# Performance work log

Hardware: AMD Instinct MI355X
Metric: run time of the kernel (lower is better)

The kernel has to match this reference:

```python
import jax, jax.numpy as jnp
import numpy as np
from jax import lax

B, H, W = 8, 2048, 2048

def _conv3x3(x, w):
    # x: [B,H,W,1], w: [3,3,1,1] (HWIO), SAME padding, stride 1
    return lax.conv_general_dilated(
        x, w, window_strides=(1, 1), padding='SAME',
        dimension_numbers=('NHWC', 'HWIO', 'NHWC'))

def setup_inputs() -> dict:
    key = jax.random.key(0)
    k1, k2, k3, k4, k5, k6 = jax.random.split(key, 6)
    x = jax.random.normal(k1, (B, H, W, 1), dtype=jnp.float32)
    mask = jax.random.randint(k2, (B, H, W, 1), 0, 2, dtype=jnp.int32)
    w1 = jax.random.normal(k3, (3, 3, 1, 1), dtype=jnp.float32)
    b1 = jax.random.normal(k4, (1,), dtype=jnp.float32)
    w2 = jax.random.normal(k5, (3, 3, 1, 1), dtype=jnp.float32)
    b2 = jax.random.normal(k6, (1,), dtype=jnp.float32)
    return {"x": x, "mask": mask, "w1": w1, "b1": b1, "w2": w2, "b2": b2}

def reference(x, mask, w1, b1, w2, b2):
    # Stride-1 MinkowskiConvolution on a sparse 2D tensor == dense 3x3 conv over
    # features zeroed at unoccupied coords, with bias + output restricted to the
    # occupied coordinate set (out_coords == in_coords for stride 1).
    m = mask.astype(x.dtype)                       # occupancy [B,H,W,1]
    h = (_conv3x3(x * m, w1) + b1) * m             # conv1 + bias on active coords
    h = jax.nn.relu(h)                             # MinkowskiReLU (per active coord)
    out = (_conv3x3(h, w2) + b2) * m               # conv2 + bias on active coords
    return out
```

## Files before the change

### kernel.cpp

```cpp
#include <hip/hip_runtime.h>


#define TB_W 128
#define TB_H 16
#define SX   136
#define SY   20
#define NV4  (SX / 4)
#define NSTG (SY * NV4)
#define HR   18
#define NQR  33
#define NQ   (HR * NQR)
#define IMG_W 2048
#define IMG_H 2048

__global__ __launch_bounds__(256) void fused_mconv2(
    const float* __restrict__ x, const int* __restrict__ mask,
    const float* __restrict__ w1p, const float* __restrict__ b1p,
    const float* __restrict__ w2p, const float* __restrict__ b2p,
    float* __restrict__ out)
{
    __shared__ __align__(16) float s_xm[SY][SX];
    __shared__ __align__(16) float s_hm[HR][SX];
    __shared__ __align__(4)  unsigned char s_mb[HR][SX];

    const int hw   = (blockIdx.z * gridDim.y + blockIdx.y) * gridDim.x + blockIdx.x;
    const int xcd  = hw & 7;
    const int slot = hw >> 3;
    const int orig = (xcd << 11) + slot;
    const int ty   = orig & 127;
    const int cl   = orig >> 7;
    const int tx   = cl & 15;
    const int tz   = cl >> 4;

    const int tid  = threadIdx.y * 64 + threadIdx.x;
    const int c0   = tx * TB_W;
    const int row0 = ty * TB_H;
    const size_t plane = (size_t)IMG_W * IMG_H;
    const float* xb = x    + (size_t)tz * plane;
    const int*   mb = mask + (size_t)tz * plane;
    float*       ob = out  + (size_t)tz * plane;

    float W1[9], W2[9];
    #pragma unroll
    for (int i = 0; i < 9; ++i) { W1[i] = w1p[i]; W2[i] = w2p[i]; }
    const float B1 = b1p[0], B2 = b2p[0];

    for (int idx = tid; idx < NSTG; idx += 256) {
        const int row  = idx / NV4;
        const int col4 = idx - row * NV4;
        const int r = row0 - 2 + row;
        const int c = c0 - 4 + (col4 << 2);
        float4 xm = make_float4(0.f, 0.f, 0.f, 0.f);
        unsigned mpack = 0u;
        if (r >= 0 && r < IMG_H && c >= 0 && c < IMG_W) {
            const size_t g = (size_t)r * IMG_W + c;
            const float4 xv = *reinterpret_cast<const float4*>(xb + g);
            const int4   mi = *reinterpret_cast<const int4*>(mb + g);
            xm.x = mi.x ? xv.x : 0.f;
            xm.y = mi.y ? xv.y : 0.f;
            xm.z = mi.z ? xv.z : 0.f;
            xm.w = mi.w ? xv.w : 0.f;
            mpack = (mi.x ? 1u : 0u) | (mi.y ? 256u : 0u) |
                    (mi.z ? 65536u : 0u) | (mi.w ? 16777216u : 0u);
        }
        *reinterpret_cast<float4*>(&s_xm[row][col4 << 2]) = xm;
        if (row >= 1 && row <= HR)
            *reinterpret_cast<unsigned*>(&s_mb[row - 1][col4 << 2]) = mpack;
    }
    __syncthreads();

    for (int idx = tid; idx < NQ; idx += 256) {
        const int hr = idx / NQR;
        const int q  = idx - hr * NQR;
        const int hc = q << 2;
        float a0 = B1, a1 = B1, a2 = B1, a3 = B1;
        #pragma unroll
        for (int di = 0; di < 3; ++di) {
            const float4 A  = *reinterpret_cast<const float4*>(&s_xm[hr + di][hc]);
            const float4 Bv = *reinterpret_cast<const float4*>(&s_xm[hr + di][hc + 4]);
            const float w0 = W1[di * 3], w1 = W1[di * 3 + 1], w2 = W1[di * 3 + 2];
            a0 += w0 * A.z  + w1 * A.w  + w2 * Bv.x;
            a1 += w0 * A.w  + w1 * Bv.x + w2 * Bv.y;
            a2 += w0 * Bv.x + w1 * Bv.y + w2 * Bv.z;
            a3 += w0 * Bv.y + w1 * Bv.z + w2 * Bv.w;
        }
        const unsigned mA = *reinterpret_cast<const unsigned*>(&s_mb[hr][hc]);
        const unsigned mB = *reinterpret_cast<const unsigned*>(&s_mb[hr][hc + 4]);
        float4 e;
        e.x = ((mA >> 24) & 255u) ? fmaxf(a0, 0.f) : -1.0f;
        e.y = ( mB        & 255u) ? fmaxf(a1, 0.f) : -1.0f;
        e.z = ((mB >>  8) & 255u) ? fmaxf(a2, 0.f) : -1.0f;
        e.w = ((mB >> 16) & 255u) ? fmaxf(a3, 0.f) : -1.0f;
        *reinterpret_cast<float4*>(&s_hm[hr][hc]) = e;
    }
    __syncthreads();

    {
        const int j     = tid & 127;
        const int strip = tid >> 7;
        const int i0    = strip * (TB_H / 2);
        float P = 0.f, Q = 0.f, cm = 0.f;
        #pragma unroll
        for (int t = 0; t < TB_H / 2 + 2; ++t) {
            const int hr = i0 + t;
            const float* rowp = &s_hm[hr][0];
            const float t0 = rowp[j];
            const float t1 = rowp[j + 1];
            const float t2 = rowp[j + 2];
            const float r0 = t0 > 0.f ? t0 : 0.f;
            const float r1 = t1 > 0.f ? t1 : 0.f;
            const float r2 = t2 > 0.f ? t2 : 0.f;
            const float d0 = W2[0] * r0 + W2[1] * r1 + W2[2] * r2;
            const float d1 = W2[3] * r0 + W2[4] * r1 + W2[5] * r2;
            const float d2 = W2[6] * r0 + W2[7] * r1 + W2[8] * r2;
            if (t >= 2) {
                const int i = i0 + t - 2;
                const float v = (cm >= 0.f) ? (Q + d2 + B2) : 0.f;
                __builtin_nontemporal_store(
                    v, ob + (size_t)(row0 + i) * IMG_W + (c0 + j));
            }
            Q  = P + d1;
            P  = d0;
            cm = t1;
        }
    }
}

extern "C" void kernel_launch(void* const* d_in, const int* in_sizes, int n_in,
                              void* d_out, int out_size, void* d_ws, size_t ws_size,
                              hipStream_t stream) {
    const float* x    = (const float*)d_in[0];
    const int*   mask = (const int*)  d_in[1];
    const float* w1   = (const float*)d_in[2];
    const float* b1   = (const float*)d_in[3];
    const float* w2   = (const float*)d_in[4];
    const float* b2   = (const float*)d_in[5];
    float*       out  = (float*)d_out;

    dim3 block(64, 4, 1);
    dim3 grid(IMG_W / TB_W, IMG_H / TB_H, 8);
    hipLaunchKernelGGL(fused_mconv2, grid, block, 0, stream,
                       x, mask, w1, b1, w2, b2, out);
}
```

Before: 72.81 us.

## Process two row bands per block with register-prefetched loads overlapping compute

Each block now handles two vertically adjacent 16-row tiles. The global loads for the second tile are issued into registers before the first tile's conv1 runs, so memory latency overlaps with compute. Shared buffers are doubled, the grid is halved to a 1D launch with XCD-aware remapping, and loads use clamped addresses so they can be issued without branching. This costs more LDS and registers per block, which may reduce occupancy, and it still reloads the halo rows shared by the two tiles.

```diff
diff --git a/kernel.cpp b/kernel.cpp
--- a/kernel.cpp
+++ b/kernel.cpp
@@ -19,22 +19,23 @@
     const float* __restrict__ w2p, const float* __restrict__ b2p,
     float* __restrict__ out)
 {
-    __shared__ __align__(16) float s_xm[SY][SX];
-    __shared__ __align__(16) float s_hm[HR][SX];
-    __shared__ __align__(4)  unsigned char s_mb[HR][SX];
+    __shared__ __align__(16) float s_xm0[SY][SX], s_xm1[SY][SX];
+    __shared__ __align__(16) float s_hm0[HR][SX], s_hm1[HR][SX];
+    __shared__ __align__(4)  unsigned char s_mb0[HR][SX], s_mb1[HR][SX];
 
-    const int hw   = (blockIdx.z * gridDim.y + blockIdx.y) * gridDim.x + blockIdx.x;
+    const int hw   = blockIdx.x;
     const int xcd  = hw & 7;
     const int slot = hw >> 3;
-    const int orig = (xcd << 11) + slot;
-    const int ty   = orig & 127;
-    const int cl   = orig >> 7;
+    const int orig = (xcd << 10) + slot;
+    const int band = orig & 63;
+    const int cl   = orig >> 6;
     const int tx   = cl & 15;
     const int tz   = cl >> 4;
 
     const int tid  = threadIdx.y * 64 + threadIdx.x;
     const int c0   = tx * TB_W;
-    const int row0 = ty * TB_H;
+    const int r0A  = band * (2 * TB_H);
+    const int r0B  = r0A + TB_H;
     const size_t plane = (size_t)IMG_W * IMG_H;
     const float* xb = x    + (size_t)tz * plane;
     const int*   mb = mask + (size_t)tz * plane;
@@ -45,57 +46,83 @@
     for (int i = 0; i < 9; ++i) { W1[i] = w1p[i]; W2[i] = w2p[i]; }
     const float B1 = b1p[0], B2 = b2p[0];
 
-    for (int idx = tid; idx < NSTG; idx += 256) {
-        const int row  = idx / NV4;
-        const int col4 = idx - row * NV4;
-        const int r = row0 - 2 + row;
-        const int c = c0 - 4 + (col4 << 2);
-        float4 xm = make_float4(0.f, 0.f, 0.f, 0.f);
-        unsigned mpack = 0u;
-        if (r >= 0 && r < IMG_H && c >= 0 && c < IMG_W) {
+    float4 xrA[3]; int4 mrA[3];
+    float4 xrB[3]; int4 mrB[3];
+    auto issue_loads = [&](int r0t, float4* xr, int4* mr) {
+        #pragma unroll
+        for (int u = 0; u < 3; ++u) {
+            const int idx  = tid + (u << 8);
+            const int cidx = idx < NSTG ? idx : NSTG - 1;
+            const int row  = cidx / NV4;
+            const int col4 = cidx - row * NV4;
+            int r = r0t - 2 + row;
+            int c = c0 - 4 + (col4 << 2);
+            r = r < 0 ? 0 : (r > IMG_H - 1 ? IMG_H - 1 : r);
+            c = c < 0 ? 0 : (c > IMG_W - 4 ? IMG_W - 4 : c);
             const size_t g = (size_t)r * IMG_W + c;
-            const float4 xv = *reinterpret_cast<const float4*>(xb + g);
-            const int4   mi = *reinterpret_cast<const int4*>(mb + g);
-            xm.x = mi.x ? xv.x : 0.f;
-            xm.y = mi.y ? xv.y : 0.f;
-            xm.z = mi.z ? xv.z : 0.f;
-            xm.w = mi.w ? xv.w : 0.f;
-            mpack = (mi.x ? 1u : 0u) | (mi.y ? 256u : 0u) |
-                    (mi.z ? 65536u : 0u) | (mi.w ? 16777216u : 0u);
+            xr[u] = *reinterpret_cast<const float4*>(xb + g);
+            mr[u] = *reinterpret_cast<const int4*>(mb + g);
         }
-        *reinterpret_cast<float4*>(&s_xm[row][col4 << 2]) = xm;
-        if (row >= 1 && row <= HR)
-            *reinterpret_cast<unsigned*>(&s_mb[row - 1][col4 << 2]) = mpack;
-    }
-    __syncthreads();
+    };
 
-    for (int idx = tid; idx < NQ; idx += 256) {
-        const int hr = idx / NQR;
-        const int q  = idx - hr * NQR;
-        const int hc = q << 2;
-        float a0 = B1, a1 = B1, a2 = B1, a3 = B1;
+    auto stage_write = [&](int r0t, const float4* xr, const int4* mr,
+                           float (*sxm)[SX], unsigned char (*smb)[SX]) {
         #pragma unroll
-        for (int di = 0; di < 3; ++di) {
-            const float4 A  = *reinterpret_cast<const float4*>(&s_xm[hr + di][hc]);
-            const float4 Bv = *reinterpret_cast<const float4*>(&s_xm[hr + di][hc + 4]);
-            const float w0 = W1[di * 3], w1 = W1[di * 3 + 1], w2 = W1[di * 3 + 2];
-            a0 += w0 * A.z  + w1 * A.w  + w2 * Bv.x;
-            a1 += w0 * A.w  + w1 * Bv.x + w2 * Bv.y;
-            a2 += w0 * Bv.x + w1 * Bv.y + w2 * Bv.z;
-            a3 += w0 * Bv.y + w1 * Bv.z + w2 * Bv.w;
+        for (int u = 0; u < 3; ++u) {
+            const int idx = tid + (u << 8);
+            if (idx < NSTG) {
+                const int row  = idx / NV4;
+                const int col4 = idx - row * NV4;
+                const int r = r0t - 2 + row;
+                const int c = c0 - 4 + (col4 << 2);
+                float4 xm = make_float4(0.f, 0.f, 0.f, 0.f);
+                unsigned mpack = 0u;
+                if (r >= 0 && r < IMG_H && c >= 0 && c < IMG_W) {
+                    const float4 xv = xr[u];
+                    const int4   mi = mr[u];
+                    xm.x = mi.x ? xv.x : 0.f;
+                    xm.y = mi.y ? xv.y : 0.f;
+                    xm.z = mi.z ? xv.z : 0.f;
+                    xm.w = mi.w ? xv.w : 0.f;
+                    mpack = (mi.x ? 1u : 0u) | (mi.y ? 256u : 0u) |
+                            (mi.z ? 65536u : 0u) | (mi.w ? 16777216u : 0u);
+                }
+                *reinterpret_cast<float4*>(&sxm[row][col4 << 2]) = xm;
+                if (row >= 1 && row <= HR)
+                    *reinterpret_cast<unsigned*>(&smb[row - 1][col4 << 2]) = mpack;
+            }
         }
-        const unsigned mA = *reinterpret_cast<const unsigned*>(&s_mb[hr][hc]);
-        const unsigned mB = *reinterpret_cast<const unsigned*>(&s_mb[hr][hc + 4]);
-        float4 e;
-        e.x = ((mA >> 24) & 255u) ? fmaxf(a0, 0.f) : -1.0f;
-        e.y = ( mB        & 255u) ? fmaxf(a1, 0.f) : -1.0f;
-        e.z = ((mB >>  8) & 255u) ? fmaxf(a2, 0.f) : -1.0f;
-        e.w = ((mB >> 16) & 255u) ? fmaxf(a3, 0.f) : -1.0f;
-        *reinterpret_cast<float4*>(&s_hm[hr][hc]) = e;
-    }
-    __syncthreads();
+    };
 
-    {
+    auto conv1 = [&](const float (*sxm)[SX], float (*shm)[SX],
+                     const unsigned char (*smb)[SX]) {
+        for (int idx = tid; idx < NQ; idx += 256) {
+            const int hr = idx / NQR;
+            const int q  = idx - hr * NQR;
+            const int hc = q << 2;
+            float a0 = B1, a1 = B1, a2 = B1, a3 = B1;
+            #pragma unroll
+            for (int di = 0; di < 3; ++di) {
+                const float4 A  = *reinterpret_cast<const float4*>(&sxm[hr + di][hc]);
+                const float4 Bv = *reinterpret_cast<const float4*>(&sxm[hr + di][hc + 4]);
+                const float w0 = W1[di * 3], w1 = W1[di * 3 + 1], w2 = W1[di * 3 + 2];
+                a0 += w0 * A.z  + w1 * A.w  + w2 * Bv.x;
+                a1 += w0 * A.w  + w1 * Bv.x + w2 * Bv.y;
+                a2 += w0 * Bv.x + w1 * Bv.y + w2 * Bv.z;
+                a3 += w0 * Bv.y + w1 * Bv.z + w2 * Bv.w;
+            }
+            const unsigned mA = *reinterpret_cast<const unsigned*>(&smb[hr][hc]);
+            const unsigned mB = *reinterpret_cast<const unsigned*>(&smb[hr][hc + 4]);
+            float4 e;
+            e.x = ((mA >> 24) & 255u) ? fmaxf(a0, 0.f) : -1.0f;
+            e.y = ( mB        & 255u) ? fmaxf(a1, 0.f) : -1.0f;
+            e.z = ((mB >>  8) & 255u) ? fmaxf(a2, 0.f) : -1.0f;
+            e.w = ((mB >> 16) & 255u) ? fmaxf(a3, 0.f) : -1.0f;
+            *reinterpret_cast<float4*>(&shm[hr][hc]) = e;
+        }
+    };
+
+    auto conv2 = [&](const float (*shm)[SX], int r0t) {
         const int j     = tid & 127;
         const int strip = tid >> 7;
         const int i0    = strip * (TB_H / 2);
@@ -103,7 +130,7 @@
         #pragma unroll
         for (int t = 0; t < TB_H / 2 + 2; ++t) {
             const int hr = i0 + t;
-            const float* rowp = &s_hm[hr][0];
+            const float* rowp = &shm[hr][0];
             const float t0 = rowp[j];
             const float t1 = rowp[j + 1];
             const float t2 = rowp[j + 2];
@@ -117,13 +144,30 @@
                 const int i = i0 + t - 2;
                 const float v = (cm >= 0.f) ? (Q + d2 + B2) : 0.f;
                 __builtin_nontemporal_store(
-                    v, ob + (size_t)(row0 + i) * IMG_W + (c0 + j));
+                    v, ob + (size_t)(r0t + i) * IMG_W + (c0 + j));
             }
             Q  = P + d1;
             P  = d0;
             cm = t1;
         }
-    }
+    };
+
+    issue_loads(r0A, xrA, mrA);
+    stage_write(r0A, xrA, mrA, s_xm0, s_mb0);
+    __syncthreads();
+
+    issue_loads(r0B, xrB, mrB);
+    conv1(s_xm0, s_hm0, s_mb0);
+    __syncthreads();
+
+    conv2(s_hm0, r0A);
+    stage_write(r0B, xrB, mrB, s_xm1, s_mb1);
+    __syncthreads();
+
+    conv1(s_xm1, s_hm1, s_mb1);
+    __syncthreads();
+
+    conv2(s_hm1, r0B);
 }
 
 extern "C" void kernel_launch(void* const* d_in, const int* in_sizes, int n_in,
@@ -138,7 +182,7 @@
     float*       out  = (float*)d_out;
 
     dim3 block(64, 4, 1);
-    dim3 grid(IMG_W / TB_W, IMG_H / TB_H, 8);
+    dim3 grid(8192, 1, 1);
     hipLaunchKernelGGL(fused_mconv2, grid, block, 0, stream,
                        x, mask, w1, b1, w2, b2, out);
 }
```

Measured after the change: 78.82 us. +8.3%, slower.

## Store masked input tile as bf16 in LDS and vectorize conv2 output stage

Applied to the files above, without the earlier changes.

The masked input tile is packed to bf16 (round-to-nearest) in shared memory, halving its LDS footprint and read traffic in the first convolution. The second convolution is remapped so each thread computes a 4-wide column group over 2 rows, using float4 LDS reads and 16-byte nontemporal stores instead of scalar ones. This cuts LDS and store instruction counts, but the bf16 rounding of inputs lowers numerical accuracy and may break tolerance.

```diff
diff --git a/kernel.cpp b/kernel.cpp
--- a/kernel.cpp
+++ b/kernel.cpp
@@ -13,14 +13,25 @@
 #define IMG_W 2048
 #define IMG_H 2048
 
+typedef float vf4 __attribute__((ext_vector_type(4)));
+
+__device__ __forceinline__ unsigned pack_bf16_rtn(float a, float b) {
+    unsigned ua = __float_as_uint(a), ub = __float_as_uint(b);
+    ua = (ua + 0x8000u) >> 16;
+    ub = (ub + 0x8000u) & 0xFFFF0000u;
+    return ua | ub;
+}
+__device__ __forceinline__ float bf_lo(unsigned u) { return __uint_as_float(u << 16); }
+__device__ __forceinline__ float bf_hi(unsigned u) { return __uint_as_float(u & 0xFFFF0000u); }
+
 __global__ __launch_bounds__(256) void fused_mconv2(
     const float* __restrict__ x, const int* __restrict__ mask,
     const float* __restrict__ w1p, const float* __restrict__ b1p,
     const float* __restrict__ w2p, const float* __restrict__ b2p,
     float* __restrict__ out)
 {
-    __shared__ __align__(16) float s_xm[SY][SX];
-    __shared__ __align__(16) float s_hm[HR][SX];
+    __shared__ __align__(16) unsigned s_xm[SY][SX / 2];
+    __shared__ __align__(16) float    s_hm[HR][SX];
     __shared__ __align__(4)  unsigned char s_mb[HR][SX];
 
     const int hw   = (blockIdx.z * gridDim.y + blockIdx.y) * gridDim.x + blockIdx.x;
@@ -63,7 +74,10 @@
             mpack = (mi.x ? 1u : 0u) | (mi.y ? 256u : 0u) |
                     (mi.z ? 65536u : 0u) | (mi.w ? 16777216u : 0u);
         }
-        *reinterpret_cast<float4*>(&s_xm[row][col4 << 2]) = xm;
+        uint2 p;
+        p.x = pack_bf16_rtn(xm.x, xm.y);
+        p.y = pack_bf16_rtn(xm.z, xm.w);
+        *reinterpret_cast<uint2*>(&s_xm[row][col4 << 1]) = p;
         if (row >= 1 && row <= HR)
             *reinterpret_cast<unsigned*>(&s_mb[row - 1][col4 << 2]) = mpack;
     }
@@ -76,13 +90,17 @@
         float a0 = B1, a1 = B1, a2 = B1, a3 = B1;
         #pragma unroll
         for (int di = 0; di < 3; ++di) {
-            const float4 A  = *reinterpret_cast<const float4*>(&s_xm[hr + di][hc]);
-            const float4 Bv = *reinterpret_cast<const float4*>(&s_xm[hr + di][hc + 4]);
+            const unsigned* xr = &s_xm[hr + di][q << 1];
+            const uint2 A  = *reinterpret_cast<const uint2*>(xr);
+            const uint2 Bv = *reinterpret_cast<const uint2*>(xr + 2);
+            const float c2 = bf_lo(A.y),  c3 = bf_hi(A.y);
+            const float c4 = bf_lo(Bv.x), c5 = bf_hi(Bv.x);
+            const float c6 = bf_lo(Bv.y), c7 = bf_hi(Bv.y);
             const float w0 = W1[di * 3], w1 = W1[di * 3 + 1], w2 = W1[di * 3 + 2];
-            a0 += w0 * A.z  + w1 * A.w  + w2 * Bv.x;
-            a1 += w0 * A.w  + w1 * Bv.x + w2 * Bv.y;
-            a2 += w0 * Bv.x + w1 * Bv.y + w2 * Bv.z;
-            a3 += w0 * Bv.y + w1 * Bv.z + w2 * Bv.w;
+            a0 += w0 * c2 + w1 * c3 + w2 * c4;
+            a1 += w0 * c3 + w1 * c4 + w2 * c5;
+            a2 += w0 * c4 + w1 * c5 + w2 * c6;
+            a3 += w0 * c5 + w1 * c6 + w2 * c7;
         }
         const unsigned mA = *reinterpret_cast<const unsigned*>(&s_mb[hr][hc]);
         const unsigned mB = *reinterpret_cast<const unsigned*>(&s_mb[hr][hc + 4]);
@@ -96,32 +114,48 @@
     __syncthreads();
 
     {
-        const int j     = tid & 127;
-        const int strip = tid >> 7;
-        const int i0    = strip * (TB_H / 2);
-        float P = 0.f, Q = 0.f, cm = 0.f;
+        const int q     = tid & 31;
+        const int strip = tid >> 5;
+        const int i0    = strip << 1;
+        const int jc    = q << 2;
+        float P[4] = {0,0,0,0}, Q[4] = {0,0,0,0}, cm[4] = {0,0,0,0};
         #pragma unroll
-        for (int t = 0; t < TB_H / 2 + 2; ++t) {
+        for (int t = 0; t < 4; ++t) {
             const int hr = i0 + t;
-            const float* rowp = &s_hm[hr][0];
-            const float t0 = rowp[j];
-            const float t1 = rowp[j + 1];
-            const float t2 = rowp[j + 2];
-            const float r0 = t0 > 0.f ? t0 : 0.f;
-            const float r1 = t1 > 0.f ? t1 : 0.f;
-            const float r2 = t2 > 0.f ? t2 : 0.f;
-            const float d0 = W2[0] * r0 + W2[1] * r1 + W2[2] * r2;
-            const float d1 = W2[3] * r0 + W2[4] * r1 + W2[5] * r2;
-            const float d2 = W2[6] * r0 + W2[7] * r1 + W2[8] * r2;
+            const float4 E1 = *reinterpret_cast<const float4*>(&s_hm[hr][jc]);
+            const float4 E2 = *reinterpret_cast<const float4*>(&s_hm[hr][jc + 4]);
+            const float v0 = E1.x, v1 = E1.y, v2 = E1.z, v3 = E1.w;
+            const float v4 = E2.x, v5 = E2.y;
+            const float r0 = fmaxf(v0, 0.f), r1 = fmaxf(v1, 0.f);
+            const float r2 = fmaxf(v2, 0.f), r3 = fmaxf(v3, 0.f);
+            const float r4 = fmaxf(v4, 0.f), r5 = fmaxf(v5, 0.f);
+            float d0[4], d1[4], d2[4];
+            d0[0] = W2[0]*r0 + W2[1]*r1 + W2[2]*r2;
+            d0[1] = W2[0]*r1 + W2[1]*r2 + W2[2]*r3;
+            d0[2] = W2[0]*r2 + W2[1]*r3 + W2[2]*r4;
+            d0[3] = W2[0]*r3 + W2[1]*r4 + W2[2]*r5;
+            d1[0] = W2[3]*r0 + W2[4]*r1 + W2[5]*r2;
+            d1[1] = W2[3]*r1 + W2[4]*r2 + W2[5]*r3;
+            d1[2] = W2[3]*r2 + W2[4]*r3 + W2[5]*r4;
+            d1[3] = W2[3]*r3 + W2[4]*r4 + W2[5]*r5;
+            d2[0] = W2[6]*r0 + W2[7]*r1 + W2[8]*r2;
+            d2[1] = W2[6]*r1 + W2[7]*r2 + W2[8]*r3;
+            d2[2] = W2[6]*r2 + W2[7]*r3 + W2[8]*r4;
+            d2[3] = W2[6]*r3 + W2[7]*r4 + W2[8]*r5;
             if (t >= 2) {
                 const int i = i0 + t - 2;
-                const float v = (cm >= 0.f) ? (Q + d2 + B2) : 0.f;
+                vf4 o;
+                o.x = (cm[0] >= 0.f) ? (Q[0] + d2[0] + B2) : 0.f;
+                o.y = (cm[1] >= 0.f) ? (Q[1] + d2[1] + B2) : 0.f;
+                o.z = (cm[2] >= 0.f) ? (Q[2] + d2[2] + B2) : 0.f;
+                o.w = (cm[3] >= 0.f) ? (Q[3] + d2[3] + B2) : 0.f;
                 __builtin_nontemporal_store(
-                    v, ob + (size_t)(row0 + i) * IMG_W + (c0 + j));
+                    o, reinterpret_cast<vf4*>(
+                           ob + (size_t)(row0 + i) * IMG_W + (c0 + jc)));
             }
-            Q  = P + d1;
-            P  = d0;
-            cm = t1;
+            #pragma unroll
+            for (int c = 0; c < 4; ++c) { Q[c] = P[c] + d1[c]; P[c] = d0[c]; }
+            cm[0] = v1; cm[1] = v2; cm[2] = v3; cm[3] = v4;
         }
     }
 }
```

After: 71.91 us, median of 2. No clear change (-1.2%).
